# Performance work log

Measured on AMD Instinct MI355X. Metric: run time of the kernel, lower is better.

The kernel has to match this reference:

```python
import jax, jax.numpy as jnp
import numpy as np

N0 = 292864   # input (hop-2) nodes
N1 = 11264    # hop-1 nodes
B = 1024      # target nodes
F_IN, HID, OUT = 128, 256, 47
E0, E1 = 281600, 10240
H_HIT = 146432
N_CACHE, N_GLOBAL, C_FEAT = 50000, 100000, 200000
P = 2048


def setup_inputs() -> dict:
    key = jax.random.key(0)
    ks = jax.random.split(key, 20)
    perm = jax.random.permutation(ks[0], N0)
    hit_pos = perm[:H_HIT]
    miss_pos = perm[H_HIT:]
    x = jax.random.normal(ks[1], (N0 - H_HIT, F_IN), jnp.float32)
    feat_cache = jax.random.normal(ks[2], (C_FEAT, F_IN), jnp.float32)
    hit_idx = jax.random.randint(ks[3], (H_HIT,), 0, C_FEAT)
    edge_index0 = jnp.stack([jax.random.randint(ks[4], (E0,), 0, N0),
                             jax.random.randint(ks[5], (E0,), 0, N1)])
    edge_index1 = jnp.stack([jax.random.randint(ks[6], (E1,), 0, N1),
                             jax.random.randint(ks[7], (E1,), 0, B)])
    emb_cache = jax.random.normal(ks[8], (N_CACHE, HID), jnp.float32)
    emb_cache_table = jax.random.randint(ks[9], (N_GLOBAL,), 0, N_CACHE)
    push_batch_id = jax.random.randint(ks[10], (P,), 0, N1)
    push_global_id = jax.random.randint(ks[11], (P,), 0, N_GLOBAL)
    pull_batch_id = jax.random.randint(ks[12], (P,), 0, N1)
    pull_global_id = jax.random.randint(ks[13], (P,), 0, N_GLOBAL)
    W0_l = jax.random.normal(ks[14], (F_IN, HID), jnp.float32) / np.sqrt(F_IN)
    b0_l = jnp.zeros((HID,), jnp.float32)
    W0_r = jax.random.normal(ks[15], (F_IN, HID), jnp.float32) / np.sqrt(F_IN)
    W1_l = jax.random.normal(ks[16], (HID, OUT), jnp.float32) / np.sqrt(HID)
    b1_l = jnp.zeros((OUT,), jnp.float32)
    W1_r = jax.random.normal(ks[17], (HID, OUT), jnp.float32) / np.sqrt(HID)
    return dict(x=x, feat_cache=feat_cache, emb_cache=emb_cache, hit_idx=hit_idx,
                hit_pos=hit_pos, miss_pos=miss_pos, edge_index0=edge_index0,
                edge_index1=edge_index1, emb_cache_table=emb_cache_table,
                push_batch_id=push_batch_id, push_global_id=push_global_id,
                pull_batch_id=pull_batch_id, pull_global_id=pull_global_id,
                W0_l=W0_l, b0_l=b0_l, W0_r=W0_r, W1_l=W1_l, b1_l=b1_l, W1_r=W1_r)


def _sage_conv(h_src, h_dst, edge_index, n_dst, W_l, b_l, W_r):
    # PyG SAGEConv (mean aggr): out = lin_l(mean_j x_j) + lin_r(x_i)
    src, dst = edge_index[0], edge_index[1]
    msg = h_src[src]                                              # [E, F] gather
    s = jax.ops.segment_sum(msg, dst, num_segments=n_dst)        # scatter-add
    cnt = jax.ops.segment_sum(jnp.ones((src.shape[0],), h_src.dtype), dst,
                              num_segments=n_dst)[:, None]
    mean = s / jnp.maximum(cnt, 1.0)
    return mean @ W_l + b_l + h_dst @ W_r


def reference(x, feat_cache, emb_cache, hit_idx, hit_pos, miss_pos,
              edge_index0, edge_index1, emb_cache_table,
              push_batch_id, push_global_id, pull_batch_id, pull_global_id,
              W0_l, b0_l, W0_r, W1_l, b1_l, W1_r):
    # Assemble node features from pinned feature cache (hits) + fetched feats (misses)
    h = jnp.zeros((N0, F_IN), x.dtype)
    h = h.at[hit_pos].set(feat_cache[hit_idx]).at[miss_pos].set(x)
    # Layer 0 (inner hop)
    h = _sage_conv(h, h[:N1], edge_index0, N1, W0_l, b0_l, W0_r)
    h = jax.nn.relu(h)  # dropout p=0.5 skipped (eval mode)
    # Last layer: push stale embeddings into cache, then pull cached embeddings
    slots_push = emb_cache_table[push_global_id]
    emb_cache = emb_cache.at[slots_push].set(jax.lax.stop_gradient(h[push_batch_id]))
    pulled = jax.lax.stop_gradient(emb_cache[emb_cache_table[pull_global_id]])
    h = h.at[pull_batch_id].set(pulled)
    out = _sage_conv(h, h[:B], edge_index1, B, W1_l, b1_l, W1_r)
    return jax.nn.log_softmax(out, axis=-1)
```

## Files before the change

kernel.cpp:

```cpp
#include <hip/hip_runtime.h>
#include <math.h>

#define N0c     292864
#define N1c     11264
#define Bc      1024
#define F_INc   128
#define HIDc    256
#define OUTc    47
#define E0c     281600
#define E1c     10240
#define H_HITc  146432
#define N_CACHEc 50000
#define C_FEATc 200000
#define Pc      2048

__global__ void prep_kernel(const int* __restrict__ hit_pos, const int* __restrict__ hit_idx,
                            const int* __restrict__ miss_pos, int* __restrict__ map,
                            int* __restrict__ cur0, int* __restrict__ pwin,
                            int* __restrict__ cur1, int* __restrict__ win) {
  int i = blockIdx.x * 256 + threadIdx.x;
  if (i < H_HITc) {
    map[hit_pos[i]]  = hit_idx[i];
    map[miss_pos[i]] = C_FEATc + i;
  }
  if (i < N1c) { cur0[i] = 0; pwin[i] = -1; }
  if (i < Bc)  cur1[i] = 0;
  if (i < N_CACHEc) win[i] = -1;
}

__global__ void deg_both_kernel(const int* __restrict__ e0, const int* __restrict__ e1,
                                int* __restrict__ deg0, int* __restrict__ deg1) {
  int i = blockIdx.x * 256 + threadIdx.x;
  if (i < E0c) {
    atomicAdd(&deg0[e0[E0c + i]], 1);
  } else if (i < E0c + E1c) {
    int j = i - E0c;
    atomicAdd(&deg1[e1[E1c + j]], 1);
  }
}

__device__ void scan_block(const int* __restrict__ deg, int* __restrict__ off,
                           int* __restrict__ cur, int n) {
  __shared__ int wsum[16];
  int tid = threadIdx.x;
  int lane = tid & 63, wid = tid >> 6;
  int ITEMS = (n + 1023) >> 10;
  int base = tid * ITEMS;
  int v[12];
  int sum = 0;
  for (int j = 0; j < ITEMS; ++j) {
    int i = base + j;
    v[j] = (i < n) ? deg[i] : 0;
    sum += v[j];
  }
  int s = sum;
  for (int o = 1; o < 64; o <<= 1) {
    int t = __shfl_up(s, o);
    if (lane >= o) s += t;
  }
  if (lane == 63) wsum[wid] = s;
  __syncthreads();
  if (tid < 16) {
    int w = wsum[tid];
    for (int o = 1; o < 16; o <<= 1) {
      int t = __shfl_up(w, o);
      if (tid >= o) w += t;
    }
    wsum[tid] = w;
  }
  __syncthreads();
  int wbase = (wid > 0) ? wsum[wid - 1] : 0;
  int run = wbase + s - sum;
  for (int j = 0; j < ITEMS; ++j) {
    int i = base + j;
    if (i < n) { off[i] = run; cur[i] = run; run += v[j]; }
  }
  if (tid == 1023) off[n] = run;
}

__global__ __launch_bounds__(1024) void scan_both_kernel(
    int* __restrict__ cur0, int* __restrict__ off0,
    int* __restrict__ cur1, int* __restrict__ off1) {
  if (blockIdx.x == 0) scan_block(cur0, off0, cur0, N1c);
  else                 scan_block(cur1, off1, cur1, Bc);
}

__global__ void scatter_both_kernel(const int* __restrict__ e0, const int* __restrict__ e1,
                                    const int* __restrict__ map,
                                    int* __restrict__ cur0, int* __restrict__ esrc0,
                                    int* __restrict__ cur1, int* __restrict__ esrc1) {
  int i = blockIdx.x * 256 + threadIdx.x;
  if (i < E0c) {
    int p = atomicAdd(&cur0[e0[E0c + i]], 1);
    esrc0[p] = map[e0[i]];
  } else if (i < E0c + E1c) {
    int j = i - E0c;
    int p = atomicAdd(&cur1[e1[E1c + j]], 1);
    esrc1[p] = e1[j];
  }
}

__global__ __launch_bounds__(256) void agg1_kernel(
    const int* __restrict__ off, const int* __restrict__ esrc,
    const float* __restrict__ fc, const float* __restrict__ x,
    float4* __restrict__ mean4) {
  __shared__ float4 sbuf[8][32];
  int d = blockIdx.x;
  int slot = threadIdx.x >> 5, lane = threadIdx.x & 31;
  int s = off[d], e = off[d + 1];
  float4 acc = make_float4(0.f, 0.f, 0.f, 0.f);
  int i = s + slot;
  int m = (i < e) ? esrc[i] : -1;
  while (i < e) {
    int inext = i + 8;
    int mnext = (inext < e) ? esrc[inext] : -1;
    const float* row = (m < C_FEATc) ? (fc + (size_t)m * F_INc)
                                     : (x + (size_t)(m - C_FEATc) * F_INc);
    float4 v = ((const float4*)row)[lane];
    acc.x += v.x; acc.y += v.y; acc.z += v.z; acc.w += v.w;
    i = inext; m = mnext;
  }
  sbuf[slot][lane] = acc;
  __syncthreads();
  if (slot < 4) {
    float4 o = sbuf[slot + 4][lane];
    acc.x += o.x; acc.y += o.y; acc.z += o.z; acc.w += o.w;
    sbuf[slot][lane] = acc;
  }
  __syncthreads();
  if (slot < 2) {
    float4 o = sbuf[slot + 2][lane];
    acc.x += o.x; acc.y += o.y; acc.z += o.z; acc.w += o.w;
    sbuf[slot][lane] = acc;
  }
  __syncthreads();
  if (slot == 0) {
    float4 o = sbuf[1][lane];
    acc.x += o.x; acc.y += o.y; acc.z += o.z; acc.w += o.w;
    float inv = 1.f / fmaxf((float)(e - s), 1.f);
    float4 r = make_float4(acc.x * inv, acc.y * inv, acc.z * inv, acc.w * inv);
    mean4[(size_t)d * 32 + lane] = r;
  }
}

#define ROWS1 16
__global__ __launch_bounds__(256) void gemm1_kernel(
    const float4* __restrict__ mean4, const int* __restrict__ map,
    const float* __restrict__ fc, const float* __restrict__ x,
    const float* __restrict__ W0l, const float* __restrict__ b0,
    const float* __restrict__ W0r, float* __restrict__ h1) {
  __shared__ float lin[ROWS1][256];
  int g0 = blockIdx.x * ROWS1;
  int tid = threadIdx.x;
  for (int idx = tid; idx < ROWS1 * 32; idx += 256) {
    int r = idx >> 5, l = idx & 31;
    ((float4*)&lin[r][0])[l] = mean4[(size_t)(g0 + r) * 32 + l];
  }
  for (int idx = tid; idx < ROWS1 * 32; idx += 256) {
    int r = idx >> 5, l = idx & 31;
    int m = map[g0 + r];
    const float* row = (m < C_FEATc) ? (fc + (size_t)m * F_INc)
                                     : (x + (size_t)(m - C_FEATc) * F_INc);
    ((float4*)&lin[r][128])[l] = ((const float4*)row)[l];
  }
  __syncthreads();
  int col = tid;
  float acc[ROWS1];
#pragma unroll
  for (int r = 0; r < ROWS1; ++r) acc[r] = 0.f;
  for (int kb = 0; kb < 32; ++kb) {
    float w0 = W0l[(kb * 4 + 0) * 256 + col];
    float w1 = W0l[(kb * 4 + 1) * 256 + col];
    float w2 = W0l[(kb * 4 + 2) * 256 + col];
    float w3 = W0l[(kb * 4 + 3) * 256 + col];
#pragma unroll
    for (int r = 0; r < ROWS1; ++r) {
      float4 a = *(const float4*)&lin[r][kb * 4];
      acc[r] += a.x * w0 + a.y * w1 + a.z * w2 + a.w * w3;
    }
  }
  for (int kb = 0; kb < 32; ++kb) {
    float w0 = W0r[(kb * 4 + 0) * 256 + col];
    float w1 = W0r[(kb * 4 + 1) * 256 + col];
    float w2 = W0r[(kb * 4 + 2) * 256 + col];
    float w3 = W0r[(kb * 4 + 3) * 256 + col];
#pragma unroll
    for (int r = 0; r < ROWS1; ++r) {
      float4 a = *(const float4*)&lin[r][128 + kb * 4];
      acc[r] += a.x * w0 + a.y * w1 + a.z * w2 + a.w * w3;
    }
  }
  float b = b0[col];
#pragma unroll
  for (int r = 0; r < ROWS1; ++r) {
    float v = acc[r] + b;
    h1[(size_t)(g0 + r) * HIDc + col] = v > 0.f ? v : 0.f;
  }
}

__global__ void win_both_kernel(const int* __restrict__ push_gid, const int* __restrict__ table,
                                int* __restrict__ win,
                                const int* __restrict__ pull_bid, int* __restrict__ pwin) {
  int i = blockIdx.x * 256 + threadIdx.x;
  if (i < Pc) atomicMax(&win[table[push_gid[i]]], i);
  else if (i < 2 * Pc) {
    int j = i - Pc;
    atomicMax(&pwin[pull_bid[j]], j);
  }
}

__global__ void pull_gather_kernel(const int* __restrict__ pull_bid, const int* __restrict__ pull_gid,
                                   const int* __restrict__ table, const int* __restrict__ win,
                                   const int* __restrict__ pwin, const int* __restrict__ push_bid,
                                   const float* __restrict__ h1, const float* __restrict__ emb_cache,
                                   float* __restrict__ pulled) {
  int i = blockIdx.x;
  int t = threadIdx.x;
  if (pwin[pull_bid[i]] != i) return;
  int slot = table[pull_gid[i]];
  int j = win[slot];
  const float* src = (j >= 0) ? (h1 + (size_t)push_bid[j] * HIDc)
                              : (emb_cache + (size_t)slot * HIDc);
  pulled[(size_t)i * HIDc + t] = src[t];
}

__global__ void pull_apply_kernel(const int* __restrict__ pull_bid, const int* __restrict__ pwin,
                                  const float* __restrict__ pulled, float* __restrict__ h1) {
  int i = blockIdx.x;
  int t = threadIdx.x;
  if (pwin[pull_bid[i]] != i) return;
  h1[(size_t)pull_bid[i] * HIDc + t] = pulled[(size_t)i * HIDc + t];
}

__global__ __launch_bounds__(256) void conv2_kernel(
    const int* __restrict__ off, const int* __restrict__ esrc,
    const float* __restrict__ h1,
    const float* __restrict__ W1l, const float* __restrict__ b1,
    const float* __restrict__ W1r, float* __restrict__ out) {
  __shared__ float lin[512];
  __shared__ float partial[64][4];
  int row = blockIdx.x;
  int t = threadIdx.x;
  int s = off[row], e = off[row + 1];
  float acc = 0.f;
  for (int i = s; i < e; ++i) acc += h1[(size_t)esrc[i] * HIDc + t];
  lin[t] = acc / fmaxf((float)(e - s), 1.f);
  lin[256 + t] = h1[(size_t)row * HIDc + t];
  __syncthreads();
  int col = t >> 2;
  int seg = t & 3;
  float p = 0.f;
  if (col < OUTc) {
    int k0 = seg * 64;
    for (int k = k0; k < k0 + 64; ++k) p += lin[k] * W1l[k * OUTc + col];
    for (int k = k0; k < k0 + 64; ++k) p += lin[256 + k] * W1r[k * OUTc + col];
  }
  partial[col][seg] = p;
  __syncthreads();
  if (t < 64) {
    float v = partial[t][0] + partial[t][1] + partial[t][2] + partial[t][3];
    if (t < OUTc) v += b1[t];
    float vv = (t < OUTc) ? v : -INFINITY;
    float m = vv;
    for (int o = 32; o > 0; o >>= 1) m = fmaxf(m, __shfl_xor(m, o));
    float ex = (t < OUTc) ? expf(vv - m) : 0.f;
    float sum = ex;
    for (int o = 32; o > 0; o >>= 1) sum += __shfl_xor(sum, o);
    if (t < OUTc) out[(size_t)row * OUTc + t] = vv - m - logf(sum);
  }
}

extern "C" void kernel_launch(void* const* d_in, const int* in_sizes, int n_in,
                              void* d_out, int out_size, void* d_ws, size_t ws_size,
                              hipStream_t stream) {
  const float* x          = (const float*)d_in[0];
  const float* feat_cache = (const float*)d_in[1];
  const float* emb_cache  = (const float*)d_in[2];
  const int* hit_idx      = (const int*)d_in[3];
  const int* hit_pos      = (const int*)d_in[4];
  const int* miss_pos     = (const int*)d_in[5];
  const int* e0           = (const int*)d_in[6];
  const int* e1           = (const int*)d_in[7];
  const int* table        = (const int*)d_in[8];
  const int* push_bid     = (const int*)d_in[9];
  const int* push_gid     = (const int*)d_in[10];
  const int* pull_bid     = (const int*)d_in[11];
  const int* pull_gid     = (const int*)d_in[12];
  const float* W0l        = (const float*)d_in[13];
  const float* b0         = (const float*)d_in[14];
  const float* W0r        = (const float*)d_in[15];
  const float* W1l        = (const float*)d_in[16];
  const float* b1         = (const float*)d_in[17];
  const float* W1r        = (const float*)d_in[18];
  float* out = (float*)d_out;

  char* p = (char*)d_ws;
  size_t ob = 0;
  auto take = [&](size_t bytes) -> void* {
    void* r = p + ob;
    ob += (bytes + 255) & ~(size_t)255;
    return r;
  };
  int* MAP     = (int*)take((size_t)N0c * 4);
  int* OFF0    = (int*)take((size_t)(N1c + 1) * 4);
  int* CUR0    = (int*)take((size_t)N1c * 4);
  int* ESRC0   = (int*)take((size_t)E0c * 4);
  float* MEAN1 = (float*)take((size_t)N1c * F_INc * 4);
  float* H1    = (float*)take((size_t)N1c * HIDc * 4);
  int* WIN     = (int*)take((size_t)N_CACHEc * 4);
  int* PWIN    = (int*)take((size_t)N1c * 4);
  float* PULLED= (float*)take((size_t)Pc * HIDc * 4);
  int* OFF1    = (int*)take((size_t)(Bc + 1) * 4);
  int* CUR1    = (int*)take((size_t)Bc * 4);
  int* ESRC1   = (int*)take((size_t)E1c * 4);

  prep_kernel<<<(H_HITc + 255) / 256, 256, 0, stream>>>(hit_pos, hit_idx, miss_pos,
                                                        MAP, CUR0, PWIN, CUR1, WIN);
  deg_both_kernel<<<(E0c + E1c + 255) / 256, 256, 0, stream>>>(e0, e1, CUR0, CUR1);
  scan_both_kernel<<<2, 1024, 0, stream>>>(CUR0, OFF0, CUR1, OFF1);
  scatter_both_kernel<<<(E0c + E1c + 255) / 256, 256, 0, stream>>>(e0, e1, MAP,
                                                                  CUR0, ESRC0, CUR1, ESRC1);
  agg1_kernel<<<N1c, 256, 0, stream>>>(OFF0, ESRC0, feat_cache, x, (float4*)MEAN1);
  gemm1_kernel<<<N1c / ROWS1, 256, 0, stream>>>((const float4*)MEAN1, MAP, feat_cache, x,
                                                W0l, b0, W0r, H1);
  win_both_kernel<<<(2 * Pc + 255) / 256, 256, 0, stream>>>(push_gid, table, WIN, pull_bid, PWIN);
  pull_gather_kernel<<<Pc, HIDc, 0, stream>>>(pull_bid, pull_gid, table, WIN, PWIN,
                                              push_bid, H1, emb_cache, PULLED);
  pull_apply_kernel<<<Pc, HIDc, 0, stream>>>(pull_bid, PWIN, PULLED, H1);
  conv2_kernel<<<Bc, 256, 0, stream>>>(OFF1, ESRC1, H1, W1l, b1, W1r, out);
}
```

Before: 362.3 us.

## Replace pull gather/apply copies with row indirection and unroll agg1 edge loop

The two kernels that copied pulled embedding rows into a buffer and back into H1 are replaced by a small resolve kernel. It records, per hop-1 node, which row (from H1 or the embedding cache) supplies its features, and conv2 reads through that indirection. The agg1 gather loop is also unrolled to keep two independent row loads in flight per warp slot. This removes one kernel launch and two 2048x256 copies, at the cost of an extra index lookup per edge in conv2.

```diff
diff --git a/kernel.cpp b/kernel.cpp
--- a/kernel.cpp
+++ b/kernel.cpp
@@ -17,13 +17,14 @@
 __global__ void prep_kernel(const int* __restrict__ hit_pos, const int* __restrict__ hit_idx,
                             const int* __restrict__ miss_pos, int* __restrict__ map,
                             int* __restrict__ cur0, int* __restrict__ pwin,
-                            int* __restrict__ cur1, int* __restrict__ win) {
+                            int* __restrict__ cur1, int* __restrict__ win,
+                            int* __restrict__ src_row) {
   int i = blockIdx.x * 256 + threadIdx.x;
   if (i < H_HITc) {
     map[hit_pos[i]]  = hit_idx[i];
     map[miss_pos[i]] = C_FEATc + i;
   }
-  if (i < N1c) { cur0[i] = 0; pwin[i] = -1; }
+  if (i < N1c) { cur0[i] = 0; pwin[i] = -1; src_row[i] = i; }
   if (i < Bc)  cur1[i] = 0;
   if (i < N_CACHEc) win[i] = -1;
 }
@@ -108,38 +109,48 @@
   int d = blockIdx.x;
   int slot = threadIdx.x >> 5, lane = threadIdx.x & 31;
   int s = off[d], e = off[d + 1];
-  float4 acc = make_float4(0.f, 0.f, 0.f, 0.f);
-  int i = s + slot;
-  int m = (i < e) ? esrc[i] : -1;
-  while (i < e) {
-    int inext = i + 8;
-    int mnext = (inext < e) ? esrc[inext] : -1;
-    const float* row = (m < C_FEATc) ? (fc + (size_t)m * F_INc)
-                                     : (x + (size_t)(m - C_FEATc) * F_INc);
-    float4 v = ((const float4*)row)[lane];
-    acc.x += v.x; acc.y += v.y; acc.z += v.z; acc.w += v.w;
-    i = inext; m = mnext;
-  }
-  sbuf[slot][lane] = acc;
+  float4 acc0 = make_float4(0.f, 0.f, 0.f, 0.f);
+  float4 acc1 = make_float4(0.f, 0.f, 0.f, 0.f);
+  int i0 = s + slot, i1 = s + slot + 8;
+  int m0 = (i0 < e) ? esrc[i0] : -1;
+  int m1 = (i1 < e) ? esrc[i1] : -1;
+  while (i0 < e) {
+    int i0n = i0 + 16, i1n = i1 + 16;
+    int m0n = (i0n < e) ? esrc[i0n] : -1;
+    int m1n = (i1n < e) ? esrc[i1n] : -1;
+    const float* r0 = (m0 < C_FEATc) ? (fc + (size_t)m0 * F_INc)
+                                     : (x + (size_t)(m0 - C_FEATc) * F_INc);
+    float4 v0 = ((const float4*)r0)[lane];
+    if (i1 < e) {
+      const float* r1 = (m1 < C_FEATc) ? (fc + (size_t)m1 * F_INc)
+                                       : (x + (size_t)(m1 - C_FEATc) * F_INc);
+      float4 v1 = ((const float4*)r1)[lane];
+      acc1.x += v1.x; acc1.y += v1.y; acc1.z += v1.z; acc1.w += v1.w;
+    }
+    acc0.x += v0.x; acc0.y += v0.y; acc0.z += v0.z; acc0.w += v0.w;
+    i0 = i0n; m0 = m0n; i1 = i1n; m1 = m1n;
+  }
+  acc0.x += acc1.x; acc0.y += acc1.y; acc0.z += acc1.z; acc0.w += acc1.w;
+  sbuf[slot][lane] = acc0;
   __syncthreads();
   if (slot < 4) {
     float4 o = sbuf[slot + 4][lane];
-    acc.x += o.x; acc.y += o.y; acc.z += o.z; acc.w += o.w;
-    sbuf[slot][lane] = acc;
+    acc0.x += o.x; acc0.y += o.y; acc0.z += o.z; acc0.w += o.w;
+    sbuf[slot][lane] = acc0;
   }
   __syncthreads();
   if (slot < 2) {
     float4 o = sbuf[slot + 2][lane];
-    acc.x += o.x; acc.y += o.y; acc.z += o.z; acc.w += o.w;
-    sbuf[slot][lane] = acc;
+    acc0.x += o.x; acc0.y += o.y; acc0.z += o.z; acc0.w += o.w;
+    sbuf[slot][lane] = acc0;
   }
   __syncthreads();
   if (slot == 0) {
     float4 o = sbuf[1][lane];
-    acc.x += o.x; acc.y += o.y; acc.z += o.z; acc.w += o.w;
+    acc0.x += o.x; acc0.y += o.y; acc0.z += o.z; acc0.w += o.w;
     float inv = 1.f / fmaxf((float)(e - s), 1.f);
-    float4 r = make_float4(acc.x * inv, acc.y * inv, acc.z * inv, acc.w * inv);
-    mean4[(size_t)d * 32 + lane] = r;
+    mean4[(size_t)d * 32 + lane] = make_float4(acc0.x * inv, acc0.y * inv,
+                                               acc0.z * inv, acc0.w * inv);
   }
 }
 
@@ -209,32 +220,23 @@
   }
 }
 
-__global__ void pull_gather_kernel(const int* __restrict__ pull_bid, const int* __restrict__ pull_gid,
-                                   const int* __restrict__ table, const int* __restrict__ win,
-                                   const int* __restrict__ pwin, const int* __restrict__ push_bid,
-                                   const float* __restrict__ h1, const float* __restrict__ emb_cache,
-                                   float* __restrict__ pulled) {
-  int i = blockIdx.x;
-  int t = threadIdx.x;
-  if (pwin[pull_bid[i]] != i) return;
+__global__ void resolve_kernel(const int* __restrict__ pull_bid, const int* __restrict__ pull_gid,
+                               const int* __restrict__ table, const int* __restrict__ win,
+                               const int* __restrict__ pwin, const int* __restrict__ push_bid,
+                               int* __restrict__ src_row) {
+  int i = blockIdx.x * 256 + threadIdx.x;
+  if (i >= Pc) return;
+  int b = pull_bid[i];
+  if (pwin[b] != i) return;
   int slot = table[pull_gid[i]];
   int j = win[slot];
-  const float* src = (j >= 0) ? (h1 + (size_t)push_bid[j] * HIDc)
-                              : (emb_cache + (size_t)slot * HIDc);
-  pulled[(size_t)i * HIDc + t] = src[t];
-}
-
-__global__ void pull_apply_kernel(const int* __restrict__ pull_bid, const int* __restrict__ pwin,
-                                  const float* __restrict__ pulled, float* __restrict__ h1) {
-  int i = blockIdx.x;
-  int t = threadIdx.x;
-  if (pwin[pull_bid[i]] != i) return;
-  h1[(size_t)pull_bid[i] * HIDc + t] = pulled[(size_t)i * HIDc + t];
+  src_row[b] = (j >= 0) ? push_bid[j] : (N1c + slot);
 }
 
 __global__ __launch_bounds__(256) void conv2_kernel(
     const int* __restrict__ off, const int* __restrict__ esrc,
-    const float* __restrict__ h1,
+    const int* __restrict__ src_row,
+    const float* __restrict__ h1, const float* __restrict__ emb,
     const float* __restrict__ W1l, const float* __restrict__ b1,
     const float* __restrict__ W1r, float* __restrict__ out) {
   __shared__ float lin[512];
@@ -243,9 +245,19 @@
   int t = threadIdx.x;
   int s = off[row], e = off[row + 1];
   float acc = 0.f;
-  for (int i = s; i < e; ++i) acc += h1[(size_t)esrc[i] * HIDc + t];
+  for (int i = s; i < e; ++i) {
+    int m = src_row[esrc[i]];
+    const float* rp = (m < N1c) ? (h1 + (size_t)m * HIDc)
+                                : (emb + (size_t)(m - N1c) * HIDc);
+    acc += rp[t];
+  }
   lin[t] = acc / fmaxf((float)(e - s), 1.f);
-  lin[256 + t] = h1[(size_t)row * HIDc + t];
+  {
+    int m = src_row[row];
+    const float* rp = (m < N1c) ? (h1 + (size_t)m * HIDc)
+                                : (emb + (size_t)(m - N1c) * HIDc);
+    lin[256 + t] = rp[t];
+  }
   __syncthreads();
   int col = t >> 2;
   int seg = t & 3;
@@ -309,13 +321,13 @@
   float* H1    = (float*)take((size_t)N1c * HIDc * 4);
   int* WIN     = (int*)take((size_t)N_CACHEc * 4);
   int* PWIN    = (int*)take((size_t)N1c * 4);
-  float* PULLED= (float*)take((size_t)Pc * HIDc * 4);
+  int* SRCROW  = (int*)take((size_t)N1c * 4);
   int* OFF1    = (int*)take((size_t)(Bc + 1) * 4);
   int* CUR1    = (int*)take((size_t)Bc * 4);
   int* ESRC1   = (int*)take((size_t)E1c * 4);
 
   prep_kernel<<<(H_HITc + 255) / 256, 256, 0, stream>>>(hit_pos, hit_idx, miss_pos,
-                                                        MAP, CUR0, PWIN, CUR1, WIN);
+                                                        MAP, CUR0, PWIN, CUR1, WIN, SRCROW);
   deg_both_kernel<<<(E0c + E1c + 255) / 256, 256, 0, stream>>>(e0, e1, CUR0, CUR1);
   scan_both_kernel<<<2, 1024, 0, stream>>>(CUR0, OFF0, CUR1, OFF1);
   scatter_both_kernel<<<(E0c + E1c + 255) / 256, 256, 0, stream>>>(e0, e1, MAP,
@@ -324,8 +336,7 @@
   gemm1_kernel<<<N1c / ROWS1, 256, 0, stream>>>((const float4*)MEAN1, MAP, feat_cache, x,
                                                 W0l, b0, W0r, H1);
   win_both_kernel<<<(2 * Pc + 255) / 256, 256, 0, stream>>>(push_gid, table, WIN, pull_bid, PWIN);
-  pull_gather_kernel<<<Pc, HIDc, 0, stream>>>(pull_bid, pull_gid, table, WIN, PWIN,
-                                              push_bid, H1, emb_cache, PULLED);
-  pull_apply_kernel<<<Pc, HIDc, 0, stream>>>(pull_bid, PWIN, PULLED, H1);
-  conv2_kernel<<<Bc, 256, 0, stream>>>(OFF1, ESRC1, H1, W1l, b1, W1r, out);
-}
+  resolve_kernel<<<(Pc + 255) / 256, 256, 0, stream>>>(pull_bid, pull_gid, table, WIN,
+                                                       PWIN, push_bid, SRCROW);
+  conv2_kernel<<<Bc, 256, 0, stream>>>(OFF1, ESRC1, SRCROW, H1, emb_cache, W1l, b1, W1r, out);
+}
```

After: 353.9 us. 1.02x faster.
